# Kernel optimization log

Hardware: AMD Instinct MI355X
Metric: run time of the kernel (lower is better)

The kernel has to match this reference:

```python
import jax, jax.numpy as jnp
import numpy as np

DIM = 512
NUM_HEAD = 8
HEAD_DIM = DIM // NUM_HEAD
FFN = 4 * DIM


def setup_inputs() -> dict:
    key = jax.random.key(0)
    ks = jax.random.split(key, 16)
    s = DIM ** -0.5
    inp = {
        "x": jax.random.normal(ks[0], (4, 2048, DIM), jnp.float32),
        "wq": jax.random.normal(ks[1], (DIM, DIM), jnp.float32) * s,
        "bq": jnp.zeros((DIM,), jnp.float32),
        "wk": jax.random.normal(ks[2], (DIM, DIM), jnp.float32) * s,
        "bk": jnp.zeros((DIM,), jnp.float32),
        "wv": jax.random.normal(ks[3], (DIM, DIM), jnp.float32) * s,
        "bv": jnp.zeros((DIM,), jnp.float32),
        "wo": jax.random.normal(ks[4], (DIM, DIM), jnp.float32) * s,
        "bo": jnp.zeros((DIM,), jnp.float32),
        "w1": jax.random.normal(ks[5], (DIM, FFN), jnp.float32) * s,
        "b1": jnp.zeros((FFN,), jnp.float32),
        "w2": jax.random.normal(ks[6], (FFN, DIM), jnp.float32) * (FFN ** -0.5),
        "b2": jnp.zeros((DIM,), jnp.float32),
        "g1": jnp.ones((DIM,), jnp.float32),
        "be1": jnp.zeros((DIM,), jnp.float32),
        "g2": jnp.ones((DIM,), jnp.float32),
        "be2": jnp.zeros((DIM,), jnp.float32),
    }
    return inp


def layer_norm(x, g, b, eps=1e-5):
    mu = jnp.mean(x, axis=-1, keepdims=True)
    var = jnp.var(x, axis=-1, keepdims=True)
    return (x - mu) * jax.lax.rsqrt(var + eps) * g + b


def _forward(x, wq, bq, wk, bk, wv, bv, wo, bo, w1, b1, w2, b2, g1, be1, g2, be2):
    b, n, _ = x.shape
    scale = HEAD_DIM ** -0.5
    q = (x @ wq + bq).reshape(b, n, NUM_HEAD, HEAD_DIM).transpose(0, 2, 1, 3)
    k = (x @ wk + bk).reshape(b, n, NUM_HEAD, HEAD_DIM).transpose(0, 2, 1, 3)
    v = (x @ wv + bv).reshape(b, n, NUM_HEAD, HEAD_DIM).transpose(0, 2, 1, 3)
    scores = jnp.einsum('bhqd,bhkd->bhqk', q, k) * scale
    attn = jax.nn.softmax(scores, axis=-1)
    out = jnp.einsum('bhqk,bhkd->bhqd', attn, v)
    out = out.transpose(0, 2, 1, 3).reshape(b, n, DIM)
    out = out @ wo + bo
    x = layer_norm(out + x, g1, be1)
    h = jax.nn.gelu(x @ w1 + b1, approximate=False)
    ff = h @ w2 + b2
    x = layer_norm(ff + x, g2, be2)
    return x


def reference(x, wq, bq, wk, bk, wv, bv, wo, bo, w1, b1, w2, b2, g1, be1, g2, be2):
    return _forward(x, wq, bq, wk, bk, wv, bv, wo, bo, w1, b1, w2, b2, g1, be1, g2, be2)
```

## Files before the change

### kernel.cpp

```cpp
#include <hip/hip_runtime.h>
#include <math.h>

#define DIM 512
#define NHEAD 8
#define HD 64
#define FFN_DIM 2048
#define BATCH 4
#define SEQ 2048
#define MTOK (BATCH*SEQ)

typedef __attribute__((ext_vector_type(8))) short bf16x8;
typedef __attribute__((ext_vector_type(4))) short bf16x4;
typedef __attribute__((ext_vector_type(4))) float f32x4;

__device__ __forceinline__ unsigned short f2b(float f){
    unsigned int u = __float_as_uint(f);
    u += 0x7fffu + ((u >> 16) & 1u);
    return (unsigned short)(u >> 16);
}
__device__ __forceinline__ float b2f(unsigned short u){
    return __uint_as_float(((unsigned int)u) << 16);
}
__device__ __forceinline__ unsigned int pack_trunc(float f0, float f1){
    return __builtin_amdgcn_perm(__float_as_uint(f1), __float_as_uint(f0), 0x07060302u);
}
__device__ __forceinline__ void async_cp16(const unsigned short* g, unsigned short* l){
    __builtin_amdgcn_global_load_lds((const __attribute__((address_space(1))) unsigned int*)g,
                                     (__attribute__((address_space(3))) unsigned int*)l, 16, 0, 0);
}
__device__ __forceinline__ f32x4 mfma16(bf16x4 a, bf16x4 b, f32x4 c){
    asm("v_mfma_f32_16x16x16_bf16 %0, %1, %2, %0" : "+v"(c) : "v"(a), "v"(b));
    return c;
}
__device__ __forceinline__ float gelu_fast(float x){
    float x3 = x*x*x;
    float y  = 2.302588f * (x + 0.044715f*x3);
    float t  = __builtin_amdgcn_exp2f(y);
    return x * t * __builtin_amdgcn_rcpf(t + 1.0f);
}

__device__ __forceinline__ void transp32(const float* __restrict__ in, unsigned short* __restrict__ out,
                                         int N, int K, int n0_rd, int n0_wr, int k0,
                                         unsigned short (&t)[32][33], int tid){
    int tx = tid & 31, ty = tid >> 5;
    #pragma unroll
    for (int u = 0; u < 4; u++)
        t[tx][ty + 8*u] = f2b(in[(size_t)(k0 + ty + 8*u)*N + n0_rd + tx]);
    __syncthreads();
    #pragma unroll
    for (int u = 0; u < 4; u++)
        out[(size_t)(n0_wr + ty + 8*u)*K + k0 + tx] = t[ty + 8*u][tx];
}

__global__ void prep_kernel(const float* __restrict__ x,
                            const float* __restrict__ wq, const float* __restrict__ wk,
                            const float* __restrict__ wv, const float* __restrict__ wo,
                            const float* __restrict__ w1, const float* __restrict__ w2,
                            const float* __restrict__ bq, const float* __restrict__ bk,
                            const float* __restrict__ bv,
                            unsigned short* __restrict__ xb, unsigned short* __restrict__ wqkvT,
                            unsigned short* __restrict__ woT, unsigned short* __restrict__ w1T,
                            unsigned short* __restrict__ w2T, float* __restrict__ bqkv)
{
    __shared__ unsigned short t[32][33];
    int bid = blockIdx.x, tid = threadIdx.x;
    if (bid < 4096) {
        int i = (bid*256 + tid)*4;
        float4 v = *(const float4*)(x + i);
        ushort4 o; o.x=f2b(v.x); o.y=f2b(v.y); o.z=f2b(v.z); o.w=f2b(v.w);
        *(ushort4*)(xb + i) = o;
    } else if (bid < 4864) {
        int r = bid - 4096;
        int n0 = (r % 48)*32, k0 = (r / 48)*32;
        const float* w = (n0 < 512) ? wq : (n0 < 1024) ? wk : wv;
        transp32(w, wqkvT, 512, 512, n0 & 511, n0, k0, t, tid);
    } else if (bid < 5120) {
        int r = bid - 4864;
        int n0 = (r % 16)*32, k0 = (r / 16)*32;
        transp32(wo, woT, 512, 512, n0, n0, k0, t, tid);
    } else if (bid < 6144) {
        int r = bid - 5120;
        int n0 = (r % 64)*32, k0 = (r / 64)*32;
        transp32(w1, w1T, 2048, 512, n0, n0, k0, t, tid);
    } else if (bid < 7168) {
        int r = bid - 6144;
        int n0 = (r % 16)*32, k0 = (r / 16)*32;
        transp32(w2, w2T, 512, 2048, n0, n0, k0, t, tid);
    } else {
        int i = (bid - 7168)*256 + tid;
        if (i < 1536)
            bqkv[i] = (i < 512) ? bq[i] : (i < 1024) ? bk[i-512] : bv[i-1024];
    }
}

template<int MODE, int SK>
__global__ __launch_bounds__(256, 4)
void gemm_bf16(const unsigned short* __restrict__ A, const unsigned short* __restrict__ Bt,
               const float* __restrict__ bias,
               unsigned short* __restrict__ Cb,
               unsigned short* __restrict__ qo, unsigned short* __restrict__ ko,
               unsigned short* __restrict__ vTo,
               int M, int N, int K)
{
    __shared__ unsigned short As[128*64];
    __shared__ unsigned short Bs[128*64];
    int tid  = threadIdx.x;
    int lane = tid & 63;
    int ln = lane & 15, qd = lane >> 4;
    int m0 = blockIdx.x * 128, n0 = blockIdx.y * 128;
    int wid = tid >> 6;
    int wm = (wid >> 1) * 64;
    int wn = (wid & 1) * 64;
    int kbeg = (SK > 1) ? (int)blockIdx.z * (K/SK) : 0;
    int kend = kbeg + K/SK;
    if (SK > 1 && MODE == 0) Cb += (size_t)blockIdx.z * M * N;

    f32x4 acc[4][4];
    #pragma unroll
    for (int i = 0; i < 4; i++)
        #pragma unroll
        for (int j = 0; j < 4; j++) acc[i][j] = (f32x4){0.f,0.f,0.f,0.f};

    for (int k0 = kbeg; k0 < kend; k0 += 64) {
        #pragma unroll
        for (int i = 0; i < 4; i++) {
            int cid = i*256 + tid;
            int row = cid >> 3, cs = cid & 7;
            int cg = cs ^ (row & 7);
            async_cp16(&A[(size_t)(m0+row)*K + k0 + cg*8], &As[(cid & ~63) * 8]);
        }
        #pragma unroll
        for (int i = 0; i < 4; i++) {
            int cid = i*256 + tid;
            int row = cid >> 3, cs = cid & 7;
            int cg = cs ^ (row & 7);
            async_cp16(&Bt[(size_t)(n0+row)*K + k0 + cg*8], &Bs[(cid & ~63) * 8]);
        }
        __syncthreads();
        #pragma unroll
        for (int kk = 0; kk < 64; kk += 32) {
            int c0 = kk >> 3;
            bf16x8 af[4], bf[4];
            #pragma unroll
            for (int t = 0; t < 4; t++)
                af[t] = *(bf16x8*)&As[(wm + t*16 + ln)*64 + ((c0 + qd) ^ (ln & 7))*8];
            #pragma unroll
            for (int t = 0; t < 4; t++)
                bf[t] = *(bf16x8*)&Bs[(wn + t*16 + ln)*64 + ((c0 + qd) ^ (ln & 7))*8];
            #pragma unroll
            for (int i = 0; i < 4; i++)
                #pragma unroll
                for (int j = 0; j < 4; j++)
                    acc[i][j] = __builtin_amdgcn_mfma_f32_16x16x32_bf16(af[i], bf[j], acc[i][j], 0,0,0);
        }
        __syncthreads();
    }

    const float QSCALE = 0.18033688011112042f;
    #pragma unroll
    for (int i = 0; i < 4; i++) {
        int mb = m0 + wm + i*16 + qd*4;
        #pragma unroll
        for (int j = 0; j < 4; j++) {
            int c = n0 + wn + j*16 + ln;
            float bv_ = (SK > 1 && blockIdx.z) ? 0.f : bias[c];
            float v[4];
            #pragma unroll
            for (int r = 0; r < 4; r++) v[r] = acc[i][j][r] + bv_;
            if (MODE == 0) {
                #pragma unroll
                for (int r = 0; r < 4; r++) Cb[(size_t)(mb+r)*N + c] = f2b(v[r]);
            } else if (MODE == 2) {
                #pragma unroll
                for (int r = 0; r < 4; r++)
                    Cb[(size_t)(mb+r)*N + c] = f2b(gelu_fast(v[r]));
            } else {
                int b = mb >> 11, t0 = mb & 2047;
                if (c < 512) {
                    int h = c >> 6, hd = c & 63;
                    #pragma unroll
                    for (int r = 0; r < 4; r++)
                        qo[(((size_t)(b*8 + h))*SEQ + t0 + r)*64 + hd] = f2b(v[r] * QSCALE);
                } else if (c < 1024) {
                    int cc = c - 512, h = cc >> 6, hd = cc & 63;
                    #pragma unroll
                    for (int r = 0; r < 4; r++)
                        ko[(((size_t)(b*8 + h))*SEQ + t0 + r)*64 + hd] = f2b(v[r]);
                } else {
                    int cc = c - 1024, h = cc >> 6, hd = cc & 63;
                    ushort4 pk;
                    pk.x = f2b(v[0]); pk.y = f2b(v[1]); pk.z = f2b(v[2]); pk.w = f2b(v[3]);
                    *(ushort4*)&vTo[(((size_t)(b*8 + h))*64 + hd)*SEQ + t0] = pk;
                }
            }
        }
    }
}

__global__ __launch_bounds__(512, 4)
void attn_mfma(const unsigned short* __restrict__ Q, const unsigned short* __restrict__ K,
               const unsigned short* __restrict__ VT, unsigned short* __restrict__ O)
{
    __shared__ unsigned short lds[24576];
    int tid  = threadIdx.x;
    int wid  = tid >> 6, lane = tid & 63;
    int ln = lane & 15, qd = lane >> 4;
    int wq = wid & 3;
    int wk = wid >> 2;
    int bx = blockIdx.x;
    int qb = (bx >> 3) & 15;
    int bh = (bx & 7) + 8 * (bx >> 7);

    bf16x8 qf[2][2];
    #pragma unroll
    for (int qs = 0; qs < 2; qs++)
        #pragma unroll
        for (int kk = 0; kk < 2; kk++)
            qf[qs][kk] = *(const bf16x8*)&Q[((size_t)bh*SEQ + qb*128 + wq*32 + qs*16 + ln)*64 + kk*32 + qd*8];

    int srow = tid >> 3, scs = tid & 7, scg = scs ^ (srow & 7);
    int sdst = (tid & ~63) * 8;
    #pragma unroll
    for (int t = 0; t < 2; t++) {
        async_cp16(&K [((size_t)bh*SEQ + t*64 + srow)*64 + scg*8], &lds[t*8192 + sdst]);
        async_cp16(&VT[((size_t)bh*64 + srow)*SEQ + t*64 + scg*8], &lds[t*8192 + 4096 + sdst]);
    }

    f32x4 o[2][4];
    #pragma unroll
    for (int qs = 0; qs < 2; qs++)
        #pragma unroll
        for (int dt = 0; dt < 4; dt++) o[qs][dt] = (f32x4){0.f,0.f,0.f,0.f};
    float l_i[2] = {0.f, 0.f};

    for (int kt = 0; kt < 32; kt++) {
        if (kt < 31) { asm volatile("s_waitcnt vmcnt(2)" ::: "memory"); }
        else         { asm volatile("s_waitcnt vmcnt(0)" ::: "memory"); }
        __builtin_amdgcn_s_barrier();
        __builtin_amdgcn_sched_barrier(0);
        if (kt < 30) {
            int nb = ((kt+2) % 3) * 8192;
            async_cp16(&K [((size_t)bh*SEQ + (kt+2)*64 + srow)*64 + scg*8], &lds[nb + sdst]);
            async_cp16(&VT[((size_t)bh*64 + srow)*SEQ + (kt+2)*64 + scg*8], &lds[nb + 4096 + sdst]);
        }
        int kof = (kt % 3) * 8192;
        int vof = kof + 4096;

        bf16x8 kf[2][2];
        #pragma unroll
        for (int ntl = 0; ntl < 2; ntl++)
            #pragma unroll
            for (int kk = 0; kk < 2; kk++)
                kf[ntl][kk] = *(bf16x8*)&lds[kof + (wk*32 + ntl*16 + ln)*64 + ((kk*4 + qd) ^ (ln & 7))*8];
        f32x4 s[2][2];
        #pragma unroll
        for (int qs = 0; qs < 2; qs++)
            #pragma unroll
            for (int ntl = 0; ntl < 2; ntl++) s[qs][ntl] = (f32x4){0.f,0.f,0.f,0.f};
        __builtin_amdgcn_s_setprio(1);
        #pragma unroll
        for (int kk = 0; kk < 2; kk++) {
            #pragma unroll
            for (int ntl = 0; ntl < 2; ntl++) {
                s[0][ntl] = __builtin_amdgcn_mfma_f32_16x16x32_bf16(kf[ntl][kk], qf[0][kk], s[0][ntl], 0,0,0);
                s[1][ntl] = __builtin_amdgcn_mfma_f32_16x16x32_bf16(kf[ntl][kk], qf[1][kk], s[1][ntl], 0,0,0);
            }
        }
        __builtin_amdgcn_s_setprio(0);

        bf16x4 pf[2][2];
        #pragma unroll
        for (int qs = 0; qs < 2; qs++) {
            #pragma unroll
            for (int ntl = 0; ntl < 2; ntl++) {
                float p0 = __builtin_amdgcn_exp2f(s[qs][ntl][0]);
                float p1 = __builtin_amdgcn_exp2f(s[qs][ntl][1]);
                float p2 = __builtin_amdgcn_exp2f(s[qs][ntl][2]);
                float p3 = __builtin_amdgcn_exp2f(s[qs][ntl][3]);
                l_i[qs] += (p0 + p1) + (p2 + p3);
                uint2 pk;
                pk.x = pack_trunc(p0, p1);
                pk.y = pack_trunc(p2, p3);
                pf[qs][ntl] = __builtin_bit_cast(bf16x4, pk);
            }
        }

        __builtin_amdgcn_s_setprio(1);
        #pragma unroll
        for (int ntl = 0; ntl < 2; ntl++) {
            #pragma unroll
            for (int dt = 0; dt < 4; dt++) {
                bf16x4 vf = *(bf16x4*)&lds[vof + (dt*16 + ln)*64
                                           + ((wk*4 + ntl*2 + (qd>>1)) ^ (ln & 7))*8 + (qd & 1)*4];
                o[0][dt] = mfma16(vf, pf[0][ntl], o[0][dt]);
                o[1][dt] = mfma16(vf, pf[1][ntl], o[1][dt]);
            }
        }
        __builtin_amdgcn_s_setprio(0);
    }
    asm volatile("s_nop 7");
    asm volatile("s_nop 7");

    float l[2];
    #pragma unroll
    for (int qs = 0; qs < 2; qs++) {
        float t = l_i[qs];
        t += __shfl_xor(t, 16);
        t += __shfl_xor(t, 32);
        l[qs] = t;
    }

    __syncthreads();
    float* fl = (float*)lds;
    if (wk == 1) {
        #pragma unroll
        for (int qs = 0; qs < 2; qs++) {
            #pragma unroll
            for (int dt = 0; dt < 4; dt++)
                *(f32x4*)&fl[(((wq*2 + qs)*4 + dt)*64 + lane)*4] = o[qs][dt];
            fl[8192 + (wq*2 + qs)*64 + lane] = l[qs];
        }
    }
    __syncthreads();
    if (wk == 0) {
        int b = bh >> 3, h = bh & 7;
        #pragma unroll
        for (int qs = 0; qs < 2; qs++) {
            float lt = l[qs] + fl[8192 + (wq*2 + qs)*64 + lane];
            float linv = 1.0f / lt;
            int t = qb*128 + wq*32 + qs*16 + ln;
            #pragma unroll
            for (int dt = 0; dt < 4; dt++) {
                f32x4 po = *(f32x4*)&fl[(((wq*2 + qs)*4 + dt)*64 + lane)*4];
                ushort4 pk;
                pk.x = f2b((o[qs][dt][0] + po[0])*linv);
                pk.y = f2b((o[qs][dt][1] + po[1])*linv);
                pk.z = f2b((o[qs][dt][2] + po[2])*linv);
                pk.w = f2b((o[qs][dt][3] + po[3])*linv);
                *(ushort4*)&O[((size_t)b*SEQ + t)*DIM + h*64 + dt*16 + qd*4] = pk;
            }
        }
    }
}

__global__ void ln1_kernel(const unsigned short* __restrict__ m0b, const unsigned short* __restrict__ m1b,
                           const float* __restrict__ resp,
                           const float* __restrict__ g, const float* __restrict__ be,
                           unsigned short* __restrict__ outb)
{
    int row  = blockIdx.x*4 + (threadIdx.x >> 6);
    int lane = threadIdx.x & 63;
    size_t base = (size_t)row * DIM + lane*8;

    ushort4 a0 = *(const ushort4*)(m0b + base);
    ushort4 a1 = *(const ushort4*)(m0b + base + 4);
    ushort4 c0 = *(const ushort4*)(m1b + base);
    ushort4 c1 = *(const ushort4*)(m1b + base + 4);
    float4 r0 = *(const float4*)(resp + base);
    float4 r1 = *(const float4*)(resp + base + 4);
    float v[8] = { b2f(a0.x)+b2f(c0.x)+r0.x, b2f(a0.y)+b2f(c0.y)+r0.y,
                   b2f(a0.z)+b2f(c0.z)+r0.z, b2f(a0.w)+b2f(c0.w)+r0.w,
                   b2f(a1.x)+b2f(c1.x)+r1.x, b2f(a1.y)+b2f(c1.y)+r1.y,
                   b2f(a1.z)+b2f(c1.z)+r1.z, b2f(a1.w)+b2f(c1.w)+r1.w };
    float s = 0.f, s2 = 0.f;
    #pragma unroll
    for (int i = 0; i < 8; i++) { s += v[i]; s2 += v[i]*v[i]; }
    #pragma unroll
    for (int d = 32; d >= 1; d >>= 1) { s += __shfl_xor(s, d); s2 += __shfl_xor(s2, d); }
    float mean = s * (1.0f / DIM);
    float rstd = rsqrtf(s2 * (1.0f / DIM) - mean*mean + 1e-5f);

    float4 g0 = *(const float4*)(g + lane*8);
    float4 g1 = *(const float4*)(g + lane*8 + 4);
    float4 b0 = *(const float4*)(be + lane*8);
    float4 b1 = *(const float4*)(be + lane*8 + 4);
    float gg[8] = {g0.x,g0.y,g0.z,g0.w,g1.x,g1.y,g1.z,g1.w};
    float bb[8] = {b0.x,b0.y,b0.z,b0.w,b1.x,b1.y,b1.z,b1.w};
    float o[8];
    #pragma unroll
    for (int i = 0; i < 8; i++) o[i] = (v[i]-mean)*rstd*gg[i] + bb[i];
    ushort4 p0, p1;
    p0.x=f2b(o[0]); p0.y=f2b(o[1]); p0.z=f2b(o[2]); p0.w=f2b(o[3]);
    p1.x=f2b(o[4]); p1.y=f2b(o[5]); p1.z=f2b(o[6]); p1.w=f2b(o[7]);
    *(ushort4*)(outb + base)     = p0;
    *(ushort4*)(outb + base + 4) = p1;
}

__global__ void ln2_kernel(const unsigned short* __restrict__ m0b, const unsigned short* __restrict__ m1b,
                           const unsigned short* __restrict__ resb,
                           const float* __restrict__ g, const float* __restrict__ be,
                           float* __restrict__ outf)
{
    int row  = blockIdx.x*4 + (threadIdx.x >> 6);
    int lane = threadIdx.x & 63;
    size_t base = (size_t)row * DIM + lane*8;

    ushort4 a0 = *(const ushort4*)(m0b + base);
    ushort4 a1 = *(const ushort4*)(m0b + base + 4);
    ushort4 c0 = *(const ushort4*)(m1b + base);
    ushort4 c1 = *(const ushort4*)(m1b + base + 4);
    ushort4 rb0 = *(const ushort4*)(resb + base);
    ushort4 rb1 = *(const ushort4*)(resb + base + 4);
    float v[8] = { b2f(a0.x)+b2f(c0.x)+b2f(rb0.x), b2f(a0.y)+b2f(c0.y)+b2f(rb0.y),
                   b2f(a0.z)+b2f(c0.z)+b2f(rb0.z), b2f(a0.w)+b2f(c0.w)+b2f(rb0.w),
                   b2f(a1.x)+b2f(c1.x)+b2f(rb1.x), b2f(a1.y)+b2f(c1.y)+b2f(rb1.y),
                   b2f(a1.z)+b2f(c1.z)+b2f(rb1.z), b2f(a1.w)+b2f(c1.w)+b2f(rb1.w) };
    float s = 0.f, s2 = 0.f;
    #pragma unroll
    for (int i = 0; i < 8; i++) { s += v[i]; s2 += v[i]*v[i]; }
    #pragma unroll
    for (int d = 32; d >= 1; d >>= 1) { s += __shfl_xor(s, d); s2 += __shfl_xor(s2, d); }
    float mean = s * (1.0f / DIM);
    float rstd = rsqrtf(s2 * (1.0f / DIM) - mean*mean + 1e-5f);

    float4 g0 = *(const float4*)(g + lane*8);
    float4 g1 = *(const float4*)(g + lane*8 + 4);
    float4 b0 = *(const float4*)(be + lane*8);
    float4 b1 = *(const float4*)(be + lane*8 + 4);
    float gg[8] = {g0.x,g0.y,g0.z,g0.w,g1.x,g1.y,g1.z,g1.w};
    float bb[8] = {b0.x,b0.y,b0.z,b0.w,b1.x,b1.y,b1.z,b1.w};
    float o[8];
    #pragma unroll
    for (int i = 0; i < 8; i++) o[i] = (v[i] - mean)*rstd*gg[i] + bb[i];
    *(float4*)(outf + base)     = (float4){o[0],o[1],o[2],o[3]};
    *(float4*)(outf + base + 4) = (float4){o[4],o[5],o[6],o[7]};
}

extern "C" void kernel_launch(void* const* d_in, const int* in_sizes, int n_in,
                              void* d_out, int out_size, void* d_ws, size_t ws_size,
                              hipStream_t stream) {
    const float* x   = (const float*)d_in[0];
    const float* wq  = (const float*)d_in[1];
    const float* bq  = (const float*)d_in[2];
    const float* wk  = (const float*)d_in[3];
    const float* bk  = (const float*)d_in[4];
    const float* wv  = (const float*)d_in[5];
    const float* bv  = (const float*)d_in[6];
    const float* wo  = (const float*)d_in[7];
    const float* bo  = (const float*)d_in[8];
    const float* w1  = (const float*)d_in[9];
    const float* b1  = (const float*)d_in[10];
    const float* w2  = (const float*)d_in[11];
    const float* b2  = (const float*)d_in[12];
    const float* g1  = (const float*)d_in[13];
    const float* be1 = (const float*)d_in[14];
    const float* g2  = (const float*)d_in[15];
    const float* be2 = (const float*)d_in[16];
    float* out = (float*)d_out;

    char* w = (char*)d_ws;
    size_t off = 0;
    auto alloc = [&](size_t bytes){ void* p = w + off; off += (bytes + 255) & ~(size_t)255; return p; };
    unsigned short* xb     = (unsigned short*)alloc((size_t)MTOK*DIM*2);
    unsigned short* wqkvT  = (unsigned short*)alloc((size_t)1536*512*2);
    unsigned short* woT    = (unsigned short*)alloc((size_t)512*512*2);
    unsigned short* w1T    = (unsigned short*)alloc((size_t)2048*512*2);
    unsigned short* w2T    = (unsigned short*)alloc((size_t)512*2048*2);
    float*          bqkv   = (float*)alloc(1536*4);
    unsigned short* qb_    = (unsigned short*)alloc((size_t)32*SEQ*64*2);
    unsigned short* kb_    = (unsigned short*)alloc((size_t)32*SEQ*64*2);
    unsigned short* vT_    = (unsigned short*)alloc((size_t)32*64*SEQ*2);
    unsigned short* attno  = (unsigned short*)alloc((size_t)MTOK*DIM*2);
    unsigned short* x1b    = (unsigned short*)alloc((size_t)MTOK*DIM*2);
    unsigned short* h_     = (unsigned short*)alloc((size_t)MTOK*FFN_DIM*2);
    unsigned short* ffb    = (unsigned short*)alloc((size_t)2*MTOK*DIM*2);

    prep_kernel<<<7174, 256, 0, stream>>>(x, wq, wk, wv, wo, w1, w2, bq, bk, bv,
                                          xb, wqkvT, woT, w1T, w2T, bqkv);

    gemm_bf16<1,1><<<dim3(64,12), 256, 0, stream>>>(xb, wqkvT, bqkv, nullptr,
                                                    qb_, kb_, vT_, MTOK, 1536, DIM);
    attn_mfma<<<512, 512, 0, stream>>>(qb_, kb_, vT_, attno);
    gemm_bf16<0,2><<<dim3(64,4,2), 256, 0, stream>>>(attno, woT, bo, ffb,
                                                     nullptr, nullptr, nullptr, MTOK, DIM, DIM);
    ln1_kernel<<<MTOK/4, 256, 0, stream>>>(ffb, ffb + (size_t)MTOK*DIM, x, g1, be1, x1b);
    gemm_bf16<2,1><<<dim3(64,16), 256, 0, stream>>>(x1b, w1T, b1, h_,
                                                    nullptr, nullptr, nullptr, MTOK, FFN_DIM, DIM);
    gemm_bf16<0,2><<<dim3(64,4,2), 256, 0, stream>>>(h_, w2T, b2, ffb,
                                                     nullptr, nullptr, nullptr, MTOK, DIM, FFN_DIM);
    ln2_kernel<<<MTOK/4, 256, 0, stream>>>(ffb, ffb + (size_t)MTOK*DIM, x1b, g2, be2, out);
}
```

Baseline: 240.8 us.

## Unroll attention loop by three and merge PV into 16x16x32 MFMAs

The attention key loop is unrolled three times to match the triple-buffered LDS ring, so buffer offsets become compile-time constants and the LDS address arithmetic is hoisted into precomputed per-lane pointers. The P·V product now packs two 16-key tiles into one bf16x8 operand and issues the 16x16x32 MFMA instead of pairs of inline-asm 16x16x16 MFMAs, halving the PV instruction count. It also drops the trailing s_nop padding. The larger unrolled body raises code size and register pressure. The V operand is now built from two separate 8-byte LDS reads, and its k-index ordering must line up with the P packing for the result to stay correct.

Result: slower. 310.3 us (+28.8%).

```diff
diff --git a/kernel.cpp b/kernel.cpp
--- a/kernel.cpp
+++ b/kernel.cpp
@@ -12,6 +12,8 @@
 typedef __attribute__((ext_vector_type(8))) short bf16x8;
 typedef __attribute__((ext_vector_type(4))) short bf16x4;
 typedef __attribute__((ext_vector_type(4))) float f32x4;
+typedef __attribute__((ext_vector_type(2))) unsigned int u32x2;
+typedef __attribute__((ext_vector_type(4))) unsigned int u32x4;
 
 __device__ __forceinline__ unsigned short f2b(float f){
     unsigned int u = __float_as_uint(f);
@@ -27,10 +29,6 @@
 __device__ __forceinline__ void async_cp16(const unsigned short* g, unsigned short* l){
     __builtin_amdgcn_global_load_lds((const __attribute__((address_space(1))) unsigned int*)g,
                                      (__attribute__((address_space(3))) unsigned int*)l, 16, 0, 0);
-}
-__device__ __forceinline__ f32x4 mfma16(bf16x4 a, bf16x4 b, f32x4 c){
-    asm("v_mfma_f32_16x16x16_bf16 %0, %1, %2, %0" : "+v"(c) : "v"(a), "v"(b));
-    return c;
 }
 __device__ __forceinline__ float gelu_fast(float x){
     float x3 = x*x*x;
@@ -197,6 +195,64 @@
     }
 }
 
+#define ATTN_BODY(KT_, KOF_, PREF_, VMC_)                                               \
+  {                                                                                     \
+    asm volatile("s_waitcnt vmcnt(" #VMC_ ")" ::: "memory");                            \
+    __builtin_amdgcn_s_barrier();                                                       \
+    __builtin_amdgcn_sched_barrier(0);                                                  \
+    if (PREF_) {                                                                        \
+      const int nb = (KOF_ + 16384) % 24576;                                            \
+      async_cp16(&K [((size_t)bh*SEQ + ((KT_)+2)*64 + srow)*64 + scg*8], &lds[nb + sdst]); \
+      async_cp16(&VT[((size_t)bh*64 + srow)*SEQ + ((KT_)+2)*64 + scg*8], &lds[nb + 4096 + sdst]); \
+    }                                                                                   \
+    bf16x8 kf[2][2];                                                                    \
+    _Pragma("unroll")                                                                   \
+    for (int ntl = 0; ntl < 2; ntl++) {                                                 \
+      kf[ntl][0] = *(const bf16x8*)&kp0[(KOF_) + ntl*1024];                             \
+      kf[ntl][1] = *(const bf16x8*)&kp1[(KOF_) + ntl*1024];                             \
+    }                                                                                   \
+    f32x4 s[2][2];                                                                      \
+    _Pragma("unroll")                                                                   \
+    for (int qs = 0; qs < 2; qs++)                                                      \
+      _Pragma("unroll")                                                                 \
+      for (int ntl = 0; ntl < 2; ntl++) s[qs][ntl] = (f32x4){0.f,0.f,0.f,0.f};          \
+    __builtin_amdgcn_s_setprio(1);                                                      \
+    _Pragma("unroll")                                                                   \
+    for (int kk = 0; kk < 2; kk++) {                                                    \
+      _Pragma("unroll")                                                                 \
+      for (int ntl = 0; ntl < 2; ntl++) {                                               \
+        s[0][ntl] = __builtin_amdgcn_mfma_f32_16x16x32_bf16(kf[ntl][kk], qf[0][kk], s[0][ntl], 0,0,0); \
+        s[1][ntl] = __builtin_amdgcn_mfma_f32_16x16x32_bf16(kf[ntl][kk], qf[1][kk], s[1][ntl], 0,0,0); \
+      }                                                                                 \
+    }                                                                                   \
+    __builtin_amdgcn_s_setprio(0);                                                      \
+    bf16x8 pf[2];                                                                       \
+    _Pragma("unroll")                                                                   \
+    for (int qs = 0; qs < 2; qs++) {                                                    \
+      float p[8];                                                                       \
+      _Pragma("unroll")                                                                 \
+      for (int ntl = 0; ntl < 2; ntl++)                                                 \
+        _Pragma("unroll")                                                               \
+        for (int r = 0; r < 4; r++) p[ntl*4+r] = __builtin_amdgcn_exp2f(s[qs][ntl][r]); \
+      l_i[qs] += ((p[0]+p[1])+(p[2]+p[3])) + ((p[4]+p[5])+(p[6]+p[7]));                 \
+      u32x4 pu;                                                                         \
+      pu[0] = pack_trunc(p[0], p[1]); pu[1] = pack_trunc(p[2], p[3]);                   \
+      pu[2] = pack_trunc(p[4], p[5]); pu[3] = pack_trunc(p[6], p[7]);                   \
+      pf[qs] = __builtin_bit_cast(bf16x8, pu);                                          \
+    }                                                                                   \
+    __builtin_amdgcn_s_setprio(1);                                                      \
+    _Pragma("unroll")                                                                   \
+    for (int dt = 0; dt < 4; dt++) {                                                    \
+      u32x2 va = *(const u32x2*)&vpA[(KOF_) + 4096 + dt*1024];                          \
+      u32x2 vb = *(const u32x2*)&vpB[(KOF_) + 4096 + dt*1024];                          \
+      u32x4 vv; vv[0] = va[0]; vv[1] = va[1]; vv[2] = vb[0]; vv[3] = vb[1];             \
+      bf16x8 vf = __builtin_bit_cast(bf16x8, vv);                                       \
+      o[0][dt] = __builtin_amdgcn_mfma_f32_16x16x32_bf16(vf, pf[0], o[0][dt], 0,0,0);   \
+      o[1][dt] = __builtin_amdgcn_mfma_f32_16x16x32_bf16(vf, pf[1], o[1][dt], 0,0,0);   \
+    }                                                                                   \
+    __builtin_amdgcn_s_setprio(0);                                                      \
+  }
+
 __global__ __launch_bounds__(512, 4)
 void attn_mfma(const unsigned short* __restrict__ Q, const unsigned short* __restrict__ K,
                const unsigned short* __restrict__ VT, unsigned short* __restrict__ O)
@@ -226,6 +282,11 @@
         async_cp16(&VT[((size_t)bh*64 + srow)*SEQ + t*64 + scg*8], &lds[t*8192 + 4096 + sdst]);
     }
 
+    const unsigned short* kp0 = lds + wk*2048 + ln*64 + ((0*4 + qd) ^ (ln & 7))*8;
+    const unsigned short* kp1 = lds + wk*2048 + ln*64 + ((1*4 + qd) ^ (ln & 7))*8;
+    const unsigned short* vpA = lds + ln*64 + ((wk*4     + (qd>>1)) ^ (ln & 7))*8 + (qd & 1)*4;
+    const unsigned short* vpB = lds + ln*64 + ((wk*4 + 2 + (qd>>1)) ^ (ln & 7))*8 + (qd & 1)*4;
+
     f32x4 o[2][4];
     #pragma unroll
     for (int qs = 0; qs < 2; qs++)
@@ -233,73 +294,13 @@
         for (int dt = 0; dt < 4; dt++) o[qs][dt] = (f32x4){0.f,0.f,0.f,0.f};
     float l_i[2] = {0.f, 0.f};
 
-    for (int kt = 0; kt < 32; kt++) {
-        if (kt < 31) { asm volatile("s_waitcnt vmcnt(2)" ::: "memory"); }
-        else         { asm volatile("s_waitcnt vmcnt(0)" ::: "memory"); }
-        __builtin_amdgcn_s_barrier();
-        __builtin_amdgcn_sched_barrier(0);
-        if (kt < 30) {
-            int nb = ((kt+2) % 3) * 8192;
-            async_cp16(&K [((size_t)bh*SEQ + (kt+2)*64 + srow)*64 + scg*8], &lds[nb + sdst]);
-            async_cp16(&VT[((size_t)bh*64 + srow)*SEQ + (kt+2)*64 + scg*8], &lds[nb + 4096 + sdst]);
-        }
-        int kof = (kt % 3) * 8192;
-        int vof = kof + 4096;
-
-        bf16x8 kf[2][2];
-        #pragma unroll
-        for (int ntl = 0; ntl < 2; ntl++)
-            #pragma unroll
-            for (int kk = 0; kk < 2; kk++)
-                kf[ntl][kk] = *(bf16x8*)&lds[kof + (wk*32 + ntl*16 + ln)*64 + ((kk*4 + qd) ^ (ln & 7))*8];
-        f32x4 s[2][2];
-        #pragma unroll
-        for (int qs = 0; qs < 2; qs++)
-            #pragma unroll
-            for (int ntl = 0; ntl < 2; ntl++) s[qs][ntl] = (f32x4){0.f,0.f,0.f,0.f};
-        __builtin_amdgcn_s_setprio(1);
-        #pragma unroll
-        for (int kk = 0; kk < 2; kk++) {
-            #pragma unroll
-            for (int ntl = 0; ntl < 2; ntl++) {
-                s[0][ntl] = __builtin_amdgcn_mfma_f32_16x16x32_bf16(kf[ntl][kk], qf[0][kk], s[0][ntl], 0,0,0);
-                s[1][ntl] = __builtin_amdgcn_mfma_f32_16x16x32_bf16(kf[ntl][kk], qf[1][kk], s[1][ntl], 0,0,0);
-            }
-        }
-        __builtin_amdgcn_s_setprio(0);
-
-        bf16x4 pf[2][2];
-        #pragma unroll
-        for (int qs = 0; qs < 2; qs++) {
-            #pragma unroll
-            for (int ntl = 0; ntl < 2; ntl++) {
-                float p0 = __builtin_amdgcn_exp2f(s[qs][ntl][0]);
-                float p1 = __builtin_amdgcn_exp2f(s[qs][ntl][1]);
-                float p2 = __builtin_amdgcn_exp2f(s[qs][ntl][2]);
-                float p3 = __builtin_amdgcn_exp2f(s[qs][ntl][3]);
-                l_i[qs] += (p0 + p1) + (p2 + p3);
-                uint2 pk;
-                pk.x = pack_trunc(p0, p1);
-                pk.y = pack_trunc(p2, p3);
-                pf[qs][ntl] = __builtin_bit_cast(bf16x4, pk);
-            }
-        }
-
-        __builtin_amdgcn_s_setprio(1);
-        #pragma unroll
-        for (int ntl = 0; ntl < 2; ntl++) {
-            #pragma unroll
-            for (int dt = 0; dt < 4; dt++) {
-                bf16x4 vf = *(bf16x4*)&lds[vof + (dt*16 + ln)*64
-                                           + ((wk*4 + ntl*2 + (qd>>1)) ^ (ln & 7))*8 + (qd & 1)*4];
-                o[0][dt] = mfma16(vf, pf[0][ntl], o[0][dt]);
-                o[1][dt] = mfma16(vf, pf[1][ntl], o[1][dt]);
-            }
-        }
-        __builtin_amdgcn_s_setprio(0);
-    }
-    asm volatile("s_nop 7");
-    asm volatile("s_nop 7");
+    for (int kt3 = 0; kt3 < 30; kt3 += 3) {
+        ATTN_BODY(kt3 + 0, 0,     true, 2)
+        ATTN_BODY(kt3 + 1, 8192,  true, 2)
+        ATTN_BODY(kt3 + 2, 16384, true, 2)
+    }
+    ATTN_BODY(30, 0,    false, 2)
+    ATTN_BODY(31, 8192, false, 0)
 
     float l[2];
     #pragma unroll
```
